# Performance work log

Measured on AMD Instinct MI355X. Metric: run time of the kernel, lower is better.

The kernel has to match this reference:

```python
import jax, jax.numpy as jnp
import numpy as np

B, P, D = 64, 196, 768
HP = WP = 14
N_CLASSES = 200
C = N_CLASSES + 1
K_PROTO = 5
GAMMA = 0.999
TEMP = 0.2
EPS_SK = 0.05
SK_ITERS = 3


def l2norm(x, axis=-1, eps=1e-12):
    n = jnp.linalg.norm(x, axis=axis, keepdims=True)
    return x / jnp.maximum(n, eps)


def _safe_div(a, b):
    return a / jnp.where(b > 0, b, 1.0)


def masked_sinkhorn(L_cnk, mask):
    """Vectorized per-class Sinkhorn-Knopp over masked patch groups.
    L_cnk: [C, N, K] logits; mask: [C, N] bool (patch n belongs to class c).
    Returns Q: [C, K, N] (columns of each present class sum to 1)."""
    m = mask[:, None, :].astype(L_cnk.dtype)  # [C,1,N]
    Q = jnp.exp(jnp.transpose(L_cnk, (0, 2, 1)) / EPS_SK) * m  # [C,K,N]
    Q = _safe_div(Q, Q.sum(axis=(1, 2), keepdims=True))
    Nc = mask.sum(axis=1).astype(Q.dtype)[:, None, None]  # per-class patch count
    Nc_safe = jnp.where(Nc > 0, Nc, 1.0)
    for _ in range(SK_ITERS):
        Q = _safe_div(Q, Q.sum(axis=2, keepdims=True)) / K_PROTO  # row (prototype) norm
        Q = _safe_div(Q, Q.sum(axis=1, keepdims=True)) / Nc_safe  # col (patch) norm
    Q = Q * Nc  # undo final /Nc -> each patch column sums to 1
    return Q


def setup_inputs() -> dict:
    key = jax.random.key(0)
    k1, k2, k3, k4, k5 = jax.random.split(key, 5)
    patch_tokens = jax.random.normal(k1, (B, P, D), dtype=jnp.float32)
    raw_patch_tokens = jax.random.normal(k2, (B, P, D), dtype=jnp.float32)
    prototypes = 0.02 * jax.random.normal(k3, (C, K_PROTO, D), dtype=jnp.float32)
    sa_weights = jnp.full((N_CLASSES, K_PROTO), 0.5, dtype=jnp.float32)
    pseudo_patch_labels = jax.random.randint(k5, (B, HP, WP), 0, C, dtype=jnp.int32)
    return {
        "patch_tokens": patch_tokens,
        "raw_patch_tokens": raw_patch_tokens,
        "prototypes": prototypes,
        "sa_weights": sa_weights,
        "pseudo_patch_labels": pseudo_patch_labels,
    }


def reference(patch_tokens, raw_patch_tokens, prototypes, sa_weights, pseudo_patch_labels):
    # --- patch-prototype cosine similarity ---
    pt = l2norm(patch_tokens)                       # [B,P,D]
    proto_n = l2norm(prototypes)                    # [C,K,D]
    logits = jnp.einsum('bpd,ckd->bpck', pt, proto_n)  # [B,P,C,K]
    image_logits = logits.max(axis=1)               # [B,C,K]
    # --- ScoreAggregation classifier ---
    sw = jax.nn.softmax(sa_weights, axis=-1) * K_PROTO  # [n_classes,K]
    class_logits = (image_logits[:, :-1, :] * sw).sum(-1) / TEMP  # [B,n_classes]
    # --- online clustering (detached in original) ---
    rpt = l2norm(raw_patch_tokens)
    patches_flat = rpt.reshape(-1, D)               # [N,D], N=B*P
    labels_flat = pseudo_patch_labels.reshape(-1)   # [N]
    N = labels_flat.shape[0]
    L_nck = logits.reshape(N, C, K_PROTO)
    L_cnk = jnp.transpose(L_nck, (1, 0, 2))         # [C,N,K]
    mask = labels_flat[None, :] == jnp.arange(C)[:, None]  # [C,N]
    Q = masked_sinkhorn(L_cnk, mask)                # [C,K,N]
    # grouped GEMM: P_c_new = Q_c @ I_c for every class at once
    P_new_c = jnp.einsum('ckn,nd->ckd', Q, patches_flat)  # [C,K,D]
    present = mask.any(axis=1)[:, None, None]
    P_new = jnp.where(present,
                      GAMMA * prototypes + (1.0 - GAMMA) * P_new_c,
                      prototypes)
    # part assignment: argmax_k Q[label_n, k, n] + label_n * K
    Q_nck = jnp.transpose(Q, (2, 0, 1))             # [N,C,K]
    Q_at = Q_nck[jnp.arange(N), labels_flat]        # [N,K]
    assign = jnp.argmax(Q_at, axis=-1).astype(jnp.int32) + labels_flat * K_PROTO
    part_assignment_maps = assign.reshape(B, HP * WP)
    return (logits, image_logits, class_logits, part_assignment_maps, P_new)
```

## Files before the change

kernel.cpp:

```cpp
#include <hip/hip_runtime.h>
#include <math.h>

#define B_ 64
#define P_ 196
#define D_ 768
#define C_ 201
#define K_ 5
#define N_ (B_*P_)
#define CK_ (C_*K_)
#define NPAD 1024
#define NCLS 200
#define GAMMA_ 0.999f
#define INV_TEMP 5.0f
#define INV_EPS 20.0f
#define CAP2 256
#define MTILES 98
#define ROWS_TOT (2*N_ + NPAD)

typedef short s16x8 __attribute__((ext_vector_type(8)));
typedef float f32x4 __attribute__((ext_vector_type(4)));
typedef unsigned short u16x4 __attribute__((ext_vector_type(4)));

typedef __attribute__((address_space(3))) void lds_void;
typedef __attribute__((address_space(1))) const void g_void;
#define GLD16(gp, lp) __builtin_amdgcn_global_load_lds((g_void*)(gp), (lds_void*)(lp), 16, 0, 0)

__device__ __forceinline__ unsigned short f2bf(float f) {
    unsigned int u = __float_as_uint(f);
    unsigned int r = (u + 0x7FFFu + ((u >> 16) & 1u)) >> 16;
    return (unsigned short)r;
}

__global__ __launch_bounds__(256) void norm_all_kernel(
        const float* __restrict__ patch, const float* __restrict__ rawp,
        const float* __restrict__ proto, float* __restrict__ invR,
        unsigned short* __restrict__ Abf, unsigned short* __restrict__ Bbf,
        int* __restrict__ cnt) {
    if (blockIdx.x == 0 && threadIdx.x < C_) cnt[threadIdx.x] = 0;
    int gw = blockIdx.x * 4 + (threadIdx.x >> 6);
    int lane = threadIdx.x & 63;
    const float* src; unsigned short* dst; int realR; int r; bool wantInv = false;
    if (gw < N_) { r = gw; src = patch; dst = Abf; realR = N_; }
    else if (gw < 2 * N_) { r = gw - N_; src = rawp; dst = nullptr; realR = N_; wantInv = true; }
    else { r = gw - 2 * N_; src = proto; dst = Bbf; realR = CK_; }
    unsigned short* brow = dst ? dst + (size_t)r * D_ : nullptr;
    if (r >= realR) {
        u16x4 z = (u16x4)0;
        *(u16x4*)(brow + lane * 4)       = z;
        *(u16x4*)(brow + lane * 4 + 256) = z;
        *(u16x4*)(brow + lane * 4 + 512) = z;
        return;
    }
    const float4* row4 = (const float4*)(src + (size_t)r * D_);
    float4 v0 = row4[lane], v1 = row4[lane + 64], v2 = row4[lane + 128];
    float s = v0.x*v0.x + v0.y*v0.y + v0.z*v0.z + v0.w*v0.w
            + v1.x*v1.x + v1.y*v1.y + v1.z*v1.z + v1.w*v1.w
            + v2.x*v2.x + v2.y*v2.y + v2.z*v2.z + v2.w*v2.w;
#pragma unroll
    for (int o = 1; o < 64; o <<= 1) s += __shfl_xor(s, o, 64);
    float sc = 1.f / fmaxf(sqrtf(s), 1e-12f);
    if (brow) {
        u16x4 p0 = { f2bf(v0.x*sc), f2bf(v0.y*sc), f2bf(v0.z*sc), f2bf(v0.w*sc) };
        u16x4 p1 = { f2bf(v1.x*sc), f2bf(v1.y*sc), f2bf(v1.z*sc), f2bf(v1.w*sc) };
        u16x4 p2 = { f2bf(v2.x*sc), f2bf(v2.y*sc), f2bf(v2.z*sc), f2bf(v2.w*sc) };
        *(u16x4*)(brow + lane * 4)       = p0;
        *(u16x4*)(brow + lane * 4 + 256) = p1;
        *(u16x4*)(brow + lane * 4 + 512) = p2;
    } else if (wantInv && lane == 0) invR[r] = sc;
}

#define BM 128
#define BN 128
#define BKq 32
#define KITER (D_/BKq)
#define NBUF 3
__global__ __launch_bounds__(256) void gemm_mfma_kernel(
    const unsigned short* __restrict__ Ab, const unsigned short* __restrict__ Bb,
    float* __restrict__ Cc,
    float* __restrict__ part) {
    __shared__ short As[NBUF][BM * BKq];
    __shared__ short Bs[NBUF][BN * BKq];
    __shared__ float maxw[4][2][BN];
    int tid = threadIdx.x;
    int bid = blockIdx.y * 8 + blockIdx.x;
    int swz = (bid & 7) * MTILES + (bid >> 3);
    int mtile = swz >> 3;
    int ntile = swz & 7;
    int mBase = mtile * BM;
    int nBase = ntile * BN;
    int w = tid >> 6;
    int lane = tid & 63;
    int wm = (w >> 1) * 64;
    int wn = (w & 1) * 64;
    int mrow = lane & 15;
    int kq = (lane >> 4) * 8;

    f32x4 acc[4][4];
#pragma unroll
    for (int i = 0; i < 4; ++i)
#pragma unroll
        for (int j = 0; j < 4; ++j) acc[i][j] = (f32x4)(0.f);

    int c0 = tid, c1 = tid + 256;
    const unsigned short* ga0 = Ab + (size_t)(mBase + (c0 >> 2)) * D_ + (c0 & 3) * 8;
    const unsigned short* ga1 = Ab + (size_t)(mBase + (c1 >> 2)) * D_ + (c1 & 3) * 8;
    const unsigned short* gb0 = Bb + (size_t)(nBase + (c0 >> 2)) * D_ + (c0 & 3) * 8;
    const unsigned short* gb1 = Bb + (size_t)(nBase + (c1 >> 2)) * D_ + (c1 & 3) * 8;

    auto stage = [&](int buf, int k0) {
        GLD16(ga0 + k0, &As[buf][c0 * 8]);
        GLD16(ga1 + k0, &As[buf][c1 * 8]);
        GLD16(gb0 + k0, &Bs[buf][c0 * 8]);
        GLD16(gb1 + k0, &Bs[buf][c1 * 8]);
    };

    stage(0, 0);
    stage(1, BKq);
    for (int u = 0; u < KITER; ++u) {
        if (u < KITER - 1) asm volatile("s_waitcnt vmcnt(4)" ::: "memory");
        else               asm volatile("s_waitcnt vmcnt(0)" ::: "memory");
        __builtin_amdgcn_s_barrier();
        __builtin_amdgcn_sched_barrier(0);
        if (u + 2 < KITER) stage((u + 2) % NBUF, (u + 2) * BKq);
        const short* Ac = As[u % NBUF];
        const short* Bc = Bs[u % NBUF];
        s16x8 a[4], b[4];
#pragma unroll
        for (int i = 0; i < 4; ++i)
            a[i] = *(const s16x8*)&Ac[(wm + 16 * i + mrow) * BKq + kq];
#pragma unroll
        for (int j = 0; j < 4; ++j)
            b[j] = *(const s16x8*)&Bc[(wn + 16 * j + mrow) * BKq + kq];
#pragma unroll
        for (int i = 0; i < 4; ++i)
#pragma unroll
            for (int j = 0; j < 4; ++j)
                acc[i][j] = __builtin_amdgcn_mfma_f32_16x16x32_bf16(a[i], b[j], acc[i][j], 0, 0, 0);
    }

#pragma unroll
    for (int i = 0; i < 4; ++i) {
        int gm = mBase + wm + 16 * i + (lane >> 4) * 4;
#pragma unroll
        for (int j = 0; j < 4; ++j) {
            int gn = nBase + wn + 16 * j + (lane & 15);
            if (gn < CK_) {
                Cc[(size_t)(gm + 0) * CK_ + gn] = acc[i][j][0];
                Cc[(size_t)(gm + 1) * CK_ + gn] = acc[i][j][1];
                Cc[(size_t)(gm + 2) * CK_ + gn] = acc[i][j][2];
                Cc[(size_t)(gm + 3) * CK_ + gn] = acc[i][j][3];
            }
        }
    }

    int imgA = mBase / 196;
    int rstar = 196 * (imgA + 1);
#pragma unroll
    for (int j = 0; j < 4; ++j) {
        float m0 = -INFINITY, m1 = -INFINITY;
#pragma unroll
        for (int i = 0; i < 4; ++i) {
            int gm = mBase + wm + 16 * i + (lane >> 4) * 4;
#pragma unroll
            for (int r = 0; r < 4; ++r) {
                float v = acc[i][j][r];
                if (gm + r >= rstar) m1 = fmaxf(m1, v); else m0 = fmaxf(m0, v);
            }
        }
        m0 = fmaxf(m0, __shfl_xor(m0, 16)); m0 = fmaxf(m0, __shfl_xor(m0, 32));
        m1 = fmaxf(m1, __shfl_xor(m1, 16)); m1 = fmaxf(m1, __shfl_xor(m1, 32));
        if (lane < 16) {
            maxw[w][0][wn + 16 * j + lane] = m0;
            maxw[w][1][wn + 16 * j + lane] = m1;
        }
    }
    __syncthreads();
    int s = tid >> 7, col = tid & 127, h = col >> 6;
    float vmax = fmaxf(maxw[h][s][col], maxw[h + 2][s][col]);
    part[(size_t)(mtile * 2 + s) * 1024 + nBase + col] = vmax;
}

__global__ __launch_bounds__(256) void post_kernel(
        const float* __restrict__ part, const float* __restrict__ saw,
        float* __restrict__ img, float* __restrict__ cls,
        const float* __restrict__ L, const int* __restrict__ labels,
        int* __restrict__ cnt, int* __restrict__ idxList, float* __restrict__ EList) {
    __shared__ float simg[CK_];
    if (blockIdx.x < B_) {
        int b = blockIdx.x;
        int t0 = (196 * b) >> 7;
        int t1 = (196 * b + 195) >> 7;
        for (int n = threadIdx.x; n < CK_; n += 256) {
            float m = -INFINITY;
            for (int t = t0; t <= t1; ++t) {
                int iA = (t << 7) / 196;
                int s = (iA == b) ? 0 : 1;
                m = fmaxf(m, part[(size_t)(t * 2 + s) * 1024 + n]);
            }
            img[b * CK_ + n] = m;
            simg[n] = m;
        }
        __syncthreads();
        int c = threadIdx.x;
        if (c < NCLS) {
            float w[K_];
            float mx = -INFINITY;
#pragma unroll
            for (int k = 0; k < K_; ++k) { w[k] = saw[c * K_ + k]; mx = fmaxf(mx, w[k]); }
            float ssum = 0.f;
#pragma unroll
            for (int k = 0; k < K_; ++k) { w[k] = expf(w[k] - mx); ssum += w[k]; }
            float acc = 0.f;
#pragma unroll
            for (int k = 0; k < K_; ++k)
                acc += simg[c * K_ + k] * (w[k] / ssum * (float)K_);
            cls[b * NCLS + c] = acc * INV_TEMP;
        }
    } else {
        int n = (blockIdx.x - B_) * 256 + threadIdx.x;
        if (n >= N_) return;
        int c = labels[n];
        int slot = atomicAdd(&cnt[c], 1);
        if (slot < CAP2) {
            idxList[c * CAP2 + slot] = n;
            const float* lp = L + (size_t)n * CK_ + c * K_;
#pragma unroll
            for (int k = 0; k < K_; ++k)
                EList[((size_t)(c * K_ + k)) * CAP2 + slot] = expf(lp[k] * INV_EPS);
        }
    }
}

#define NJ (CAP2/64)
__global__ __launch_bounds__(256) void sinkema_kernel(
    const int* __restrict__ cnt, const int* __restrict__ idxList,
    const float* __restrict__ EList, const float* __restrict__ invR,
    const float* __restrict__ rawP, const float* __restrict__ proto,
    float* __restrict__ outAssign, float* __restrict__ outProto) {
    int c = blockIdx.x;
    int tid = threadIdx.x;
    int Nc = cnt[c]; if (Nc > CAP2) Nc = CAP2;
    size_t protoOff = (size_t)c * K_ * D_;
    if (Nc == 0) {
        for (int i = tid; i < K_ * D_; i += 256)
            outProto[protoOff + i] = proto[protoOff + i];
        return;
    }
    __shared__ float s_w[K_][CAP2];
    __shared__ int s_idx[CAP2];
    for (int i = tid; i < CAP2; i += 256)
        s_idx[i] = (i < Nc) ? idxList[c * CAP2 + i] : 0;

    if (tid < 64) {
        int lane = tid;
        float e[NJ][K_];
        float cn[NJ];
#pragma unroll
        for (int j = 0; j < NJ; ++j) {
            int n = j * 64 + lane;
            bool v = n < Nc;
            cn[j] = v ? 1.f : 0.f;
#pragma unroll
            for (int k = 0; k < K_; ++k)
                e[j][k] = v ? EList[((size_t)(c * K_ + k)) * CAP2 + n] : 0.f;
        }
        float r[K_];
        for (int it = 0; it < 3; ++it) {
#pragma unroll
            for (int k = 0; k < K_; ++k) {
                float s = 0.f;
#pragma unroll
                for (int j = 0; j < NJ; ++j) s += e[j][k] * cn[j];
                for (int o = 32; o > 0; o >>= 1) s += __shfl_xor(s, o, 64);
                r[k] = 1.f / ((float)K_ * s);
            }
#pragma unroll
            for (int j = 0; j < NJ; ++j) {
                float t = 0.f;
#pragma unroll
                for (int k = 0; k < K_; ++k) t += e[j][k] * r[k];
                cn[j] = (j * 64 + lane < Nc) ? 1.f / ((float)Nc * t) : 0.f;
            }
        }
#pragma unroll
        for (int j = 0; j < NJ; ++j) {
            int n = j * 64 + lane;
            if (n >= Nc) continue;
            int idxn = idxList[c * CAP2 + n];
            int kb = 0; float best = e[j][0] * r[0];
#pragma unroll
            for (int k = 1; k < K_; ++k) {
                float v = e[j][k] * r[k];
                if (v > best) { best = v; kb = k; }
            }
            outAssign[idxn] = (float)(kb + c * K_);
            float scale = cn[j] * (float)Nc * (1.0f - GAMMA_) * invR[idxn];
#pragma unroll
            for (int k = 0; k < K_; ++k)
                s_w[k][n] = e[j][k] * r[k] * scale;
        }
    }
    __syncthreads();

    float a0[K_] = {}, a1[K_] = {}, a2[K_] = {};
    for (int n = 0; n < Nc; ++n) {
        const float* rp = rawP + (size_t)s_idx[n] * D_;
        float v0 = rp[tid], v1 = rp[tid + 256], v2 = rp[tid + 512];
#pragma unroll
        for (int k = 0; k < K_; ++k) {
            float wv = s_w[k][n];
            a0[k] = fmaf(wv, v0, a0[k]);
            a1[k] = fmaf(wv, v1, a1[k]);
            a2[k] = fmaf(wv, v2, a2[k]);
        }
    }
#pragma unroll
    for (int k = 0; k < K_; ++k) {
        size_t o = protoOff + (size_t)k * D_;
        outProto[o + tid]       = fmaf(GAMMA_, proto[o + tid],       a0[k]);
        outProto[o + tid + 256] = fmaf(GAMMA_, proto[o + tid + 256], a1[k]);
        outProto[o + tid + 512] = fmaf(GAMMA_, proto[o + tid + 512], a2[k]);
    }
}

extern "C" void kernel_launch(void* const* d_in, const int* in_sizes, int n_in,
                              void* d_out, int out_size, void* d_ws, size_t ws_size,
                              hipStream_t stream) {
    (void)in_sizes; (void)n_in; (void)out_size; (void)ws_size;
    const float* patch  = (const float*)d_in[0];
    const float* rawp   = (const float*)d_in[1];
    const float* proto  = (const float*)d_in[2];
    const float* saw    = (const float*)d_in[3];
    const int*   labels = (const int*)d_in[4];

    float* out    = (float*)d_out;
    float* logits = out;
    float* img    = out + 12606720;
    float* cls    = out + 12671040;
    float* assign = out + 12683840;
    float* pnew   = out + 12696384;

    float* ws   = (float*)d_ws;
    float* invR = ws;
    unsigned short* Abf = (unsigned short*)(ws + N_);
    unsigned short* Bbf = Abf + (size_t)N_ * D_;
    int*   cnt     = (int*)(Bbf + (size_t)NPAD * D_);
    int*   idxList = cnt + 256;
    float* EList   = (float*)(idxList + C_ * CAP2);
    float* WList   = EList + (size_t)C_ * K_ * CAP2;
    float* part    = WList + (size_t)C_ * K_ * CAP2;

    norm_all_kernel<<<ROWS_TOT / 4, 256, 0, stream>>>(patch, rawp, proto, invR, Abf, Bbf, cnt);
    gemm_mfma_kernel<<<dim3(NPAD / BN, MTILES), 256, 0, stream>>>(Abf, Bbf, logits, part);
    post_kernel<<<B_ + N_ / 256, 256, 0, stream>>>(part, saw, img, cls, logits, labels,
                                                   cnt, idxList, EList);
    sinkema_kernel<<<C_, 256, 0, stream>>>(cnt, idxList, EList, invR, rawp, proto,
                                           assign, pnew);
}
```

Before: 190.5 us.

## Use 2-wave GEMM blocks with 64x128 warp tiles and XOR-swizzled LDS

The bf16 MFMA GEMM block drops from four waves to two. Each wave now computes a 64x128 output tile (4x8 MFMA accumulators) instead of 64x64, which raises register reuse of the A fragments and halves the waves per tile. The global-to-LDS chunk index is XOR-swizzled by row, and the reads apply the matching swizzle, to cut LDS bank conflicts. Each thread issues more loads per stage, so the waitcnt is raised to match. The trade-off is higher register pressure (128 accumulator floats per lane) and fewer waves available to hide latency.

```diff
diff --git a/kernel.cpp b/kernel.cpp
--- a/kernel.cpp
+++ b/kernel.cpp
@@ -74,13 +74,13 @@
 #define BKq 32
 #define KITER (D_/BKq)
 #define NBUF 3
-__global__ __launch_bounds__(256) void gemm_mfma_kernel(
+__global__ __launch_bounds__(128, 2) void gemm_mfma_kernel(
     const unsigned short* __restrict__ Ab, const unsigned short* __restrict__ Bb,
     float* __restrict__ Cc,
     float* __restrict__ part) {
     __shared__ short As[NBUF][BM * BKq];
     __shared__ short Bs[NBUF][BN * BKq];
-    __shared__ float maxw[4][2][BN];
+    __shared__ float maxw[2][2][BN];
     int tid = threadIdx.x;
     int bid = blockIdx.y * 8 + blockIdx.x;
     int swz = (bid & 7) * MTILES + (bid >> 3);
@@ -90,60 +90,69 @@
     int nBase = ntile * BN;
     int w = tid >> 6;
     int lane = tid & 63;
-    int wm = (w >> 1) * 64;
-    int wn = (w & 1) * 64;
+    int wm = w * 64;
     int mrow = lane & 15;
-    int kq = (lane >> 4) * 8;
-
-    f32x4 acc[4][4];
+    int q = lane >> 4;
+    int qx = (q ^ (mrow & 3)) * 8;
+
+    f32x4 acc[4][8];
 #pragma unroll
     for (int i = 0; i < 4; ++i)
 #pragma unroll
-        for (int j = 0; j < 4; ++j) acc[i][j] = (f32x4)(0.f);
-
-    int c0 = tid, c1 = tid + 256;
-    const unsigned short* ga0 = Ab + (size_t)(mBase + (c0 >> 2)) * D_ + (c0 & 3) * 8;
-    const unsigned short* ga1 = Ab + (size_t)(mBase + (c1 >> 2)) * D_ + (c1 & 3) * 8;
-    const unsigned short* gb0 = Bb + (size_t)(nBase + (c0 >> 2)) * D_ + (c0 & 3) * 8;
-    const unsigned short* gb1 = Bb + (size_t)(nBase + (c1 >> 2)) * D_ + (c1 & 3) * 8;
+        for (int j = 0; j < 8; ++j) acc[i][j] = (f32x4)(0.f);
+
+    const unsigned short* gA[4];
+    const unsigned short* gB[4];
+    int ldsOff[4];
+#pragma unroll
+    for (int s = 0; s < 4; ++s) {
+        int c = tid + 128 * s;
+        int row = c >> 2;
+        int cx = (c & 3) ^ (row & 3);
+        gA[s] = Ab + (size_t)(mBase + row) * D_ + cx * 8;
+        gB[s] = Bb + (size_t)(nBase + row) * D_ + cx * 8;
+        ldsOff[s] = c * 8;
+    }
 
     auto stage = [&](int buf, int k0) {
-        GLD16(ga0 + k0, &As[buf][c0 * 8]);
-        GLD16(ga1 + k0, &As[buf][c1 * 8]);
-        GLD16(gb0 + k0, &Bs[buf][c0 * 8]);
-        GLD16(gb1 + k0, &Bs[buf][c1 * 8]);
+#pragma unroll
+        for (int s = 0; s < 4; ++s) GLD16(gA[s] + k0, &As[buf][ldsOff[s]]);
+#pragma unroll
+        for (int s = 0; s < 4; ++s) GLD16(gB[s] + k0, &Bs[buf][ldsOff[s]]);
     };
 
     stage(0, 0);
     stage(1, BKq);
+    int aoff = (wm + mrow) * BKq + qx;
+    int boff = mrow * BKq + qx;
     for (int u = 0; u < KITER; ++u) {
-        if (u < KITER - 1) asm volatile("s_waitcnt vmcnt(4)" ::: "memory");
+        if (u < KITER - 1) asm volatile("s_waitcnt vmcnt(8)" ::: "memory");
         else               asm volatile("s_waitcnt vmcnt(0)" ::: "memory");
         __builtin_amdgcn_s_barrier();
         __builtin_amdgcn_sched_barrier(0);
         if (u + 2 < KITER) stage((u + 2) % NBUF, (u + 2) * BKq);
         const short* Ac = As[u % NBUF];
         const short* Bc = Bs[u % NBUF];
-        s16x8 a[4], b[4];
+        s16x8 a[4], b[8];
 #pragma unroll
         for (int i = 0; i < 4; ++i)
-            a[i] = *(const s16x8*)&Ac[(wm + 16 * i + mrow) * BKq + kq];
-#pragma unroll
-        for (int j = 0; j < 4; ++j)
-            b[j] = *(const s16x8*)&Bc[(wn + 16 * j + mrow) * BKq + kq];
+            a[i] = *(const s16x8*)&Ac[aoff + 512 * i];
+#pragma unroll
+        for (int j = 0; j < 8; ++j)
+            b[j] = *(const s16x8*)&Bc[boff + 512 * j];
 #pragma unroll
         for (int i = 0; i < 4; ++i)
 #pragma unroll
-            for (int j = 0; j < 4; ++j)
+            for (int j = 0; j < 8; ++j)
                 acc[i][j] = __builtin_amdgcn_mfma_f32_16x16x32_bf16(a[i], b[j], acc[i][j], 0, 0, 0);
     }
 
 #pragma unroll
     for (int i = 0; i < 4; ++i) {
-        int gm = mBase + wm + 16 * i + (lane >> 4) * 4;
-#pragma unroll
-        for (int j = 0; j < 4; ++j) {
-            int gn = nBase + wn + 16 * j + (lane & 15);
+        int gm = mBase + wm + 16 * i + q * 4;
+#pragma unroll
+        for (int j = 0; j < 8; ++j) {
+            int gn = nBase + 16 * j + mrow;
             if (gn < CK_) {
                 Cc[(size_t)(gm + 0) * CK_ + gn] = acc[i][j][0];
                 Cc[(size_t)(gm + 1) * CK_ + gn] = acc[i][j][1];
@@ -156,11 +165,11 @@
     int imgA = mBase / 196;
     int rstar = 196 * (imgA + 1);
 #pragma unroll
-    for (int j = 0; j < 4; ++j) {
+    for (int j = 0; j < 8; ++j) {
         float m0 = -INFINITY, m1 = -INFINITY;
 #pragma unroll
         for (int i = 0; i < 4; ++i) {
-            int gm = mBase + wm + 16 * i + (lane >> 4) * 4;
+            int gm = mBase + wm + 16 * i + q * 4;
 #pragma unroll
             for (int r = 0; r < 4; ++r) {
                 float v = acc[i][j][r];
@@ -170,14 +179,16 @@
         m0 = fmaxf(m0, __shfl_xor(m0, 16)); m0 = fmaxf(m0, __shfl_xor(m0, 32));
         m1 = fmaxf(m1, __shfl_xor(m1, 16)); m1 = fmaxf(m1, __shfl_xor(m1, 32));
         if (lane < 16) {
-            maxw[w][0][wn + 16 * j + lane] = m0;
-            maxw[w][1][wn + 16 * j + lane] = m1;
+            maxw[w][0][16 * j + lane] = m0;
+            maxw[w][1][16 * j + lane] = m1;
         }
     }
     __syncthreads();
-    int s = tid >> 7, col = tid & 127, h = col >> 6;
-    float vmax = fmaxf(maxw[h][s][col], maxw[h + 2][s][col]);
-    part[(size_t)(mtile * 2 + s) * 1024 + nBase + col] = vmax;
+#pragma unroll
+    for (int s = 0; s < 2; ++s) {
+        float vmax = fmaxf(maxw[0][s][tid], maxw[1][s][tid]);
+        part[(size_t)(mtile * 2 + s) * 1024 + nBase + tid] = vmax;
+    }
 }
 
 __global__ __launch_bounds__(256) void post_kernel(
@@ -351,7 +362,7 @@
     float* part    = WList + (size_t)C_ * K_ * CAP2;
 
     norm_all_kernel<<<ROWS_TOT / 4, 256, 0, stream>>>(patch, rawp, proto, invR, Abf, Bbf, cnt);
-    gemm_mfma_kernel<<<dim3(NPAD / BN, MTILES), 256, 0, stream>>>(Abf, Bbf, logits, part);
+    gemm_mfma_kernel<<<dim3(NPAD / BN, MTILES), 128, 0, stream>>>(Abf, Bbf, logits, part);
     post_kernel<<<B_ + N_ / 256, 256, 0, stream>>>(part, saw, img, cls, logits, labels,
                                                    cnt, idxList, EList);
     sinkema_kernel<<<C_, 256, 0, stream>>>(cnt, idxList, EList, invR, rawp, proto,
```

Measured after the change: 204.5 us. 7.3% more time.

## Widen sinkema blocks to 768 threads and pack per-slot E values contiguously

Applied to the files above, without the earlier changes.

The prototype-update kernel now launches 768 threads per class block, one per feature column, replacing 256 threads that each handled three columns. The gather loop is unrolled by four patches to keep more independent loads in flight. The exp values are stored as one padded 8-float record per slot, so each lane reads them with a float4 load plus one scalar instead of five strided loads. The assignment loop also reads the patch index from LDS instead of global memory. The wider blocks add occupancy and memory-level parallelism, at the cost of more idle threads during the single-wavefront Sinkhorn phase.

```diff
diff --git a/kernel.cpp b/kernel.cpp
--- a/kernel.cpp
+++ b/kernel.cpp
@@ -14,6 +14,7 @@
 #define INV_TEMP 5.0f
 #define INV_EPS 20.0f
 #define CAP2 256
+#define EPAD 8
 #define MTILES 98
 #define ROWS_TOT (2*N_ + NPAD)
 
@@ -224,15 +225,19 @@
         if (slot < CAP2) {
             idxList[c * CAP2 + slot] = n;
             const float* lp = L + (size_t)n * CK_ + c * K_;
-#pragma unroll
-            for (int k = 0; k < K_; ++k)
-                EList[((size_t)(c * K_ + k)) * CAP2 + slot] = expf(lp[k] * INV_EPS);
+            float e0 = expf(lp[0] * INV_EPS), e1 = expf(lp[1] * INV_EPS);
+            float e2 = expf(lp[2] * INV_EPS), e3 = expf(lp[3] * INV_EPS);
+            float e4 = expf(lp[4] * INV_EPS);
+            float* ep = EList + ((size_t)c * CAP2 + slot) * EPAD;
+            float4 v4 = { e0, e1, e2, e3 };
+            *(float4*)ep = v4;
+            ep[4] = e4;
         }
     }
 }
 
 #define NJ (CAP2/64)
-__global__ __launch_bounds__(256) void sinkema_kernel(
+__global__ __launch_bounds__(768) void sinkema_kernel(
     const int* __restrict__ cnt, const int* __restrict__ idxList,
     const float* __restrict__ EList, const float* __restrict__ invR,
     const float* __restrict__ rawP, const float* __restrict__ proto,
@@ -242,13 +247,13 @@
     int Nc = cnt[c]; if (Nc > CAP2) Nc = CAP2;
     size_t protoOff = (size_t)c * K_ * D_;
     if (Nc == 0) {
-        for (int i = tid; i < K_ * D_; i += 256)
+        for (int i = tid; i < K_ * D_; i += 768)
             outProto[protoOff + i] = proto[protoOff + i];
         return;
     }
     __shared__ float s_w[K_][CAP2];
     __shared__ int s_idx[CAP2];
-    for (int i = tid; i < CAP2; i += 256)
+    for (int i = tid; i < CAP2; i += 768)
         s_idx[i] = (i < Nc) ? idxList[c * CAP2 + i] : 0;
 
     if (tid < 64) {
@@ -260,9 +265,10 @@
             int n = j * 64 + lane;
             bool v = n < Nc;
             cn[j] = v ? 1.f : 0.f;
-#pragma unroll
-            for (int k = 0; k < K_; ++k)
-                e[j][k] = v ? EList[((size_t)(c * K_ + k)) * CAP2 + n] : 0.f;
+            const float* ep = EList + ((size_t)c * CAP2 + n) * EPAD;
+            float4 v4 = v ? *(const float4*)ep : make_float4(0.f, 0.f, 0.f, 0.f);
+            e[j][0] = v4.x; e[j][1] = v4.y; e[j][2] = v4.z; e[j][3] = v4.w;
+            e[j][4] = v ? ep[4] : 0.f;
         }
         float r[K_];
         for (int it = 0; it < 3; ++it) {
@@ -286,7 +292,7 @@
         for (int j = 0; j < NJ; ++j) {
             int n = j * 64 + lane;
             if (n >= Nc) continue;
-            int idxn = idxList[c * CAP2 + n];
+            int idxn = s_idx[n];
             int kb = 0; float best = e[j][0] * r[0];
 #pragma unroll
             for (int k = 1; k < K_; ++k) {
@@ -302,24 +308,30 @@
     }
     __syncthreads();
 
-    float a0[K_] = {}, a1[K_] = {}, a2[K_] = {};
-    for (int n = 0; n < Nc; ++n) {
-        const float* rp = rawP + (size_t)s_idx[n] * D_;
-        float v0 = rp[tid], v1 = rp[tid + 256], v2 = rp[tid + 512];
+    float acc[K_] = {};
+    int n = 0;
+    for (; n + 3 < Nc; n += 4) {
+        float v0 = rawP[(size_t)s_idx[n]     * D_ + tid];
+        float v1 = rawP[(size_t)s_idx[n + 1] * D_ + tid];
+        float v2 = rawP[(size_t)s_idx[n + 2] * D_ + tid];
+        float v3 = rawP[(size_t)s_idx[n + 3] * D_ + tid];
 #pragma unroll
         for (int k = 0; k < K_; ++k) {
-            float wv = s_w[k][n];
-            a0[k] = fmaf(wv, v0, a0[k]);
-            a1[k] = fmaf(wv, v1, a1[k]);
-            a2[k] = fmaf(wv, v2, a2[k]);
-        }
+            acc[k] = fmaf(s_w[k][n],     v0, acc[k]);
+            acc[k] = fmaf(s_w[k][n + 1], v1, acc[k]);
+            acc[k] = fmaf(s_w[k][n + 2], v2, acc[k]);
+            acc[k] = fmaf(s_w[k][n + 3], v3, acc[k]);
+        }
+    }
+    for (; n < Nc; ++n) {
+        float v0 = rawP[(size_t)s_idx[n] * D_ + tid];
+#pragma unroll
+        for (int k = 0; k < K_; ++k) acc[k] = fmaf(s_w[k][n], v0, acc[k]);
     }
 #pragma unroll
     for (int k = 0; k < K_; ++k) {
-        size_t o = protoOff + (size_t)k * D_;
-        outProto[o + tid]       = fmaf(GAMMA_, proto[o + tid],       a0[k]);
-        outProto[o + tid + 256] = fmaf(GAMMA_, proto[o + tid + 256], a1[k]);
-        outProto[o + tid + 512] = fmaf(GAMMA_, proto[o + tid + 512], a2[k]);
+        size_t o = protoOff + (size_t)k * D_ + tid;
+        outProto[o] = fmaf(GAMMA_, proto[o], acc[k]);
     }
 }
 
@@ -347,13 +359,12 @@
     int*   cnt     = (int*)(Bbf + (size_t)NPAD * D_);
     int*   idxList = cnt + 256;
     float* EList   = (float*)(idxList + C_ * CAP2);
-    float* WList   = EList + (size_t)C_ * K_ * CAP2;
-    float* part    = WList + (size_t)C_ * K_ * CAP2;
+    float* part    = EList + (size_t)2 * C_ * K_ * CAP2;
 
     norm_all_kernel<<<ROWS_TOT / 4, 256, 0, stream>>>(patch, rawp, proto, invR, Abf, Bbf, cnt);
     gemm_mfma_kernel<<<dim3(NPAD / BN, MTILES), 256, 0, stream>>>(Abf, Bbf, logits, part);
     post_kernel<<<B_ + N_ / 256, 256, 0, stream>>>(part, saw, img, cls, logits, labels,
                                                    cnt, idxList, EList);
-    sinkema_kernel<<<C_, 256, 0, stream>>>(cnt, idxList, EList, invR, rawp, proto,
+    sinkema_kernel<<<C_, 768, 0, stream>>>(cnt, idxList, EList, invR, rawp, proto,
                                            assign, pnew);
 }
```

New measurement: 189.5 us. Within noise of the previous version (-0.5%).
